# Performance work log

Measured on AMD Instinct MI355X. Metric: run time of the kernel, lower is better.

The kernel has to match this reference:

```python
import jax, jax.numpy as jnp
import numpy as np

# Module hyperparameters (init_kwargs)
N_CLASSES = 21
RADIUS = 5
SIZE = (256, 256)
SIGMA_DIST = 4.0
SIGMA_FEAT = 1.0
B, C = 8, 32


def _offsets(radius):
    """Integer (dy, dx) offsets with Euclidean distance < radius (includes (0,0))."""
    offs = []
    r = int(radius)
    for dy in range(-r + 1, r):
        for dx in range(-r + 1, r):
            if dy * dy + dx * dx < radius * radius:
                offs.append((dy, dx))
    return offs


OFFSETS = _offsets(RADIUS)  # 69 offsets for radius=5


def setup_inputs() -> dict:
    key = jax.random.key(0)
    k1, k2 = jax.random.split(key)
    H, W = SIZE
    classification = jax.random.uniform(k1, (B, N_CLASSES, H, W), dtype=jnp.float32)
    features = jax.random.normal(k2, (B, C, H, W), dtype=jnp.float32)
    return {"classification": classification, "features": features}


def reference(classification, features):
    # classification: [B, K, H, W] soft assignments S
    # features:       [B, C, H, W]
    Bb, K, H, W = classification.shape
    inv_sd2 = 1.0 / (SIGMA_DIST * SIGMA_DIST)
    inv_sf2 = 1.0 / (SIGMA_FEAT * SIGMA_FEAT)

    hs = jnp.arange(H)
    ws = jnp.arange(W)

    WS = jnp.zeros_like(classification)           # (W @ S), [B, K, H, W]
    degree = jnp.zeros((Bb, H, W), classification.dtype)

    # Loop over the small fixed set of neighbor offsets (69 for radius=5).
    for dy, dx in OFFSETS:
        f_nb = jnp.roll(features, (-dy, -dx), axis=(2, 3))
        s_nb = jnp.roll(classification, (-dy, -dx), axis=(2, 3))
        # mask out wrap-around: neighbor (h+dy, w+dx) must be in-bounds
        valid_h = (hs + dy >= 0) & (hs + dy < H)
        valid_w = (ws + dx >= 0) & (ws + dx < W)
        mask = (valid_h[:, None] & valid_w[None, :]).astype(classification.dtype)
        # Gaussian affinity: distance kernel * feature kernel
        feat_d2 = ((features - f_nb) ** 2).sum(axis=1)        # [B, H, W]
        w = jnp.exp(-(dy * dy + dx * dx) * inv_sd2 - feat_d2 * inv_sf2) * mask
        WS = WS + w[:, None] * s_nb
        degree = degree + w

    # numerator   = S^T W S : [B, K, K]
    # denominator = d^T S   : [B, K]
    num = jnp.einsum('bkhw,bjhw->bkj', classification, WS)
    den = jnp.einsum('bhw,bkhw->bk', degree, classification)
    return (num / den[:, None, :]).sum()
```

## Files before the change

kernel.cpp:

```cpp
#include <hip/hip_runtime.h>

#define HH 256
#define WW 256
#define HWPX 65536
#define BB 8
#define KK 21
#define CC 32
#define NT 8192
#define E_LOG2E 1.4426950408889634f
#define PEN -30000.0f

typedef _Float16 half2v __attribute__((ext_vector_type(2)));
typedef _Float16 half8  __attribute__((ext_vector_type(8)));
typedef float    f32x4v __attribute__((ext_vector_type(4)));
union F4H { float4 f4; half2v h[4]; half8 h8; };

__global__ __launch_bounds__(256) void prep(const float* __restrict__ cls,
                                            const float* __restrict__ feat,
                                            float4* __restrict__ fpk,
                                            float2* __restrict__ TN) {
    const int tid = blockIdx.x * 256 + threadIdx.x;
    const int b = tid >> 16;
    const int p = tid & (HWPX - 1);

    const float* cbase = cls + (size_t)b * KK * HWPX + p;
    float T = 0.f;
#pragma unroll
    for (int k = 0; k < KK; ++k) T += cbase[(size_t)k * HWPX];

    const float* src = feat + (size_t)b * CC * HWPX + p;
    float nq = 0.f;
#pragma unroll
    for (int j = 0; j < 4; ++j) {
        F4H u;
#pragma unroll
        for (int k = 0; k < 4; ++k) {
            float a  = src[(size_t)(j * 8 + 2 * k) * HWPX];
            float b2 = src[(size_t)(j * 8 + 2 * k + 1) * HWPX];
            u.h[k] = __builtin_bit_cast(half2v, __builtin_amdgcn_cvt_pkrtz(a, b2));
            nq = __builtin_amdgcn_fdot2(u.h[k], u.h[k], nq, false);
        }
        fpk[(size_t)j * (BB * HWPX) + tid] = u.f4;
    }
    TN[tid] = make_float2(T, nq);
}

__global__ __launch_bounds__(256) void affinity_mfma(const float4* __restrict__ fpk,
                                                     const float2* __restrict__ TN,
                                                     const float* __restrict__ cls,
                                                     float* __restrict__ partial) {
    __shared__ float smN[4][21], smD[4][21];
    const int L    = blockIdx.x;
    const int b    = L & 7;
    const int t    = L >> 3;
    const int xt   = t >> 6;
    const int ygrp = t & 63;
    const int wid  = threadIdx.x >> 6;
    const int lane = threadIdx.x & 63;
    const int g    = lane >> 4;
    const int c    = lane & 15;
    const int y    = ygrp * 4 + wid;
    const int x0   = xt * 16;

    const size_t bofs = (size_t)b * HWPX;
    const float4* fb  = fpk + bofs;
    const float2* tnb = TN + bofs;

    const int rowp = (y << 8) + x0;
    F4H afr; afr.f4 = fb[(size_t)g * (BB * HWPX) + rowp + c];

    float npE[4];
#pragma unroll
    for (int r = 0; r < 4; ++r) npE[r] = tnb[rowp + 4 * g + r].y * E_LOG2E;

    float cstA[2][4], cstB[2][4], cstC[2][4];
    int   voffF[2], voffT[2];
#pragma unroll
    for (int w = 0; w < 2; ++w) {
        const int w0  = w ? 12 : -4;
        const int xbu = x0 + w0 + c;
        const bool inb = (unsigned)xbu < WW;
        const int xbc = min(max(xbu, 0), WW - 1);
        voffF[w] = (g * (BB * HWPX) + xbc) * 16;
        voffT[w] = xbc * 8;
#pragma unroll
        for (int r = 0; r < 4; ++r) {
            const int dx = w0 + c - 4 * g - r;
            const int s2 = dx * dx;
            const float bp = fmaf((float)s2, -E_LOG2E / 16.f, -npE[r]);
            cstA[w][r] = (inb && s2 <= 16) ? bp : PEN;
            cstB[w][r] = (inb && s2 <= 9)  ? bp : PEN;
            cstC[w][r] = (inb && s2 <= 4)  ? bp : PEN;
        }
    }

    const f32x4v czero = {0.f, 0.f, 0.f, 0.f};
    float pdeg[4] = {0.f, 0.f, 0.f, 0.f};
    float pV[4]   = {0.f, 0.f, 0.f, 0.f};

    const char* fpkB = (const char*)fpk + bofs * 16;
    const char* tnB  = (const char*)TN + bofs * 8;

    auto body = [&](const float (&cst)[2][4], int ny, float cdy) {
        if ((unsigned)ny >= HH) return;
        const char* pF = fpkB + ((size_t)ny << 12);
        const char* pT = tnB  + ((size_t)ny << 11);
#pragma unroll
        for (int w = 0; w < 2; ++w) {
            F4H bfr; bfr.f4 = *(const float4*)(pF + voffF[w]);
            const float2 tq = *(const float2*)(pT + voffT[w]);
            f32x4v cz = __builtin_amdgcn_mfma_f32_16x16x32_f16(afr.h8, bfr.h8, czero, 0, 0, 0);
            const float t1 = fmaf(tq.y, -E_LOG2E, cdy);
#pragma unroll
            for (int r = 0; r < 4; ++r) {
                const float e2 = fmaf(cz[r], 2.f * E_LOG2E, cst[w][r] + t1);
                const float wv = __builtin_exp2f(e2);
                pdeg[r] += wv;
                pV[r]   = fmaf(wv, tq.x, pV[r]);
            }
        }
    };

#pragma unroll 1
    for (int d = -2; d <= 2; ++d)
        body(cstA, y + d, (float)(d * d) * (-E_LOG2E / 16.f));
    body(cstB, y - 3, 9.f  * (-E_LOG2E / 16.f));
    body(cstB, y + 3, 9.f  * (-E_LOG2E / 16.f));
    body(cstC, y - 4, 16.f * (-E_LOG2E / 16.f));
    body(cstC, y + 4, 16.f * (-E_LOG2E / 16.f));

#pragma unroll
    for (int m = 1; m <= 8; m <<= 1) {
#pragma unroll
        for (int r = 0; r < 4; ++r) {
            pdeg[r] += __shfl_xor(pdeg[r], m, 64);
            pV[r]   += __shfl_xor(pV[r], m, 64);
        }
    }

    float n0 = 0.f, d0 = 0.f, n1 = 0.f, d1 = 0.f;
    const float* clsb = cls + (size_t)b * KK * HWPX + rowp + 4 * g;
#pragma unroll
    for (int r = 0; r < 4; ++r) {
        const float s0 = clsb[(size_t)c * HWPX + r];
        n0 = fmaf(s0, pV[r], n0);
        d0 = fmaf(s0, pdeg[r], d0);
        if (c < 5) {
            const float s1 = clsb[(size_t)(c + 16) * HWPX + r];
            n1 = fmaf(s1, pV[r], n1);
            d1 = fmaf(s1, pdeg[r], d1);
        }
    }
#pragma unroll
    for (int m = 16; m <= 32; m <<= 1) {
        n0 += __shfl_xor(n0, m, 64);
        d0 += __shfl_xor(d0, m, 64);
        n1 += __shfl_xor(n1, m, 64);
        d1 += __shfl_xor(d1, m, 64);
    }
    if (lane < 16) {
        smN[wid][lane] = n0;
        smD[wid][lane] = d0;
        if (lane < 5) { smN[wid][16 + lane] = n1; smD[wid][16 + lane] = d1; }
    }
    __syncthreads();
    if (threadIdx.x < 2 * KK) {
        const int jq = threadIdx.x;
        const float v = (jq < KK)
            ? (smN[0][jq] + smN[1][jq] + smN[2][jq] + smN[3][jq])
            : (smD[0][jq - KK] + smD[1][jq - KK] + smD[2][jq - KK] + smD[3][jq - KK]);
        partial[(size_t)jq * NT + (size_t)b * 1024 + t] = v;
    }
}

__global__ __launch_bounds__(256) void reduce_part(const float* __restrict__ partial,
                                                   float* __restrict__ numer,
                                                   float* __restrict__ denom) {
    __shared__ float sm[4];
    const int jq = blockIdx.x;
    const int b  = blockIdx.y;
    const float* src = partial + (size_t)jq * NT + (size_t)b * 1024;
    float a = src[threadIdx.x] + src[threadIdx.x + 256]
            + src[threadIdx.x + 512] + src[threadIdx.x + 768];
#pragma unroll
    for (int off = 32; off > 0; off >>= 1) a += __shfl_down(a, off);
    if ((threadIdx.x & 63) == 0) sm[threadIdx.x >> 6] = a;
    __syncthreads();
    if (threadIdx.x == 0) {
        const float v = sm[0] + sm[1] + sm[2] + sm[3];
        if (jq < KK) numer[b * KK + jq] = v;
        else         denom[b * KK + jq - KK] = v;
    }
}

__global__ __launch_bounds__(256) void finalize(const float* __restrict__ numer,
                                                const float* __restrict__ denom,
                                                float* __restrict__ out) {
    __shared__ float sm[4];
    int i = threadIdx.x;
    float r = 0.f;
    if (i < BB * KK) r = numer[i] / denom[i];
#pragma unroll
    for (int off = 32; off > 0; off >>= 1) r += __shfl_down(r, off);
    if ((i & 63) == 0) sm[i >> 6] = r;
    __syncthreads();
    if (i == 0) out[0] = sm[0] + sm[1] + sm[2] + sm[3];
}

extern "C" void kernel_launch(void* const* d_in, const int* in_sizes, int n_in,
                              void* d_out, int out_size, void* d_ws, size_t ws_size,
                              hipStream_t stream) {
    const float* cls  = (const float*)d_in[0];
    const float* feat = (const float*)d_in[1];
    float* out = (float*)d_out;

    const size_t BHW = (size_t)BB * HWPX;
    float4* fpk     = (float4*)d_ws;
    float2* TN      = (float2*)((char*)d_ws + BHW * 64);
    float*  partial = (float*)((char*)TN + BHW * 8);
    float*  numer   = partial + (size_t)2 * KK * NT;
    float*  denom   = numer + BB * KK;

    prep<<<dim3((BB * HWPX) / 256), dim3(256), 0, stream>>>(cls, feat, fpk, TN);
    affinity_mfma<<<dim3(NT), dim3(256), 0, stream>>>(fpk, TN, cls, partial);
    reduce_part<<<dim3(2 * KK, BB), dim3(256), 0, stream>>>(partial, numer, denom);
    finalize<<<dim3(1), dim3(256), 0, stream>>>(numer, denom, out);
}
```

Before: 199.8 us.

## Retile affinity MFMA to 2x8 pixel tiles covering two rows per wave

```diff
diff --git a/kernel.cpp b/kernel.cpp
--- a/kernel.cpp
+++ b/kernel.cpp
@@ -53,45 +53,45 @@
     const int L    = blockIdx.x;
     const int b    = L & 7;
     const int t    = L >> 3;
-    const int xt   = t >> 6;
-    const int ygrp = t & 63;
     const int wid  = threadIdx.x >> 6;
     const int lane = threadIdx.x & 63;
     const int g    = lane >> 4;
     const int c    = lane & 15;
-    const int y    = ygrp * 4 + wid;
-    const int x0   = xt * 16;
+    const int idx  = t * 4 + wid;
+    const int y0   = (idx >> 5) * 2;
+    const int x0   = (idx & 31) * 8;
 
     const size_t bofs = (size_t)b * HWPX;
     const float4* fb  = fpk + bofs;
     const float2* tnb = TN + bofs;
 
-    const int rowp = (y << 8) + x0;
-    F4H afr; afr.f4 = fb[(size_t)g * (BB * HWPX) + rowp + c];
-
+    F4H afr;
+    afr.f4 = fb[(size_t)g * (BB * HWPX) + ((y0 + (c & 1)) << 8) + x0 + (c >> 1)];
+
+    int pxr[4];
     float npE[4];
 #pragma unroll
-    for (int r = 0; r < 4; ++r) npE[r] = tnb[rowp + 4 * g + r].y * E_LOG2E;
-
-    float cstA[2][4], cstB[2][4], cstC[2][4];
-    int   voffF[2], voffT[2];
-#pragma unroll
-    for (int w = 0; w < 2; ++w) {
-        const int w0  = w ? 12 : -4;
-        const int xbu = x0 + w0 + c;
-        const bool inb = (unsigned)xbu < WW;
-        const int xbc = min(max(xbu, 0), WW - 1);
-        voffF[w] = (g * (BB * HWPX) + xbc) * 16;
-        voffT[w] = xbc * 8;
-#pragma unroll
-        for (int r = 0; r < 4; ++r) {
-            const int dx = w0 + c - 4 * g - r;
-            const int s2 = dx * dx;
-            const float bp = fmaf((float)s2, -E_LOG2E / 16.f, -npE[r]);
-            cstA[w][r] = (inb && s2 <= 16) ? bp : PEN;
-            cstB[w][r] = (inb && s2 <= 9)  ? bp : PEN;
-            cstC[w][r] = (inb && s2 <= 4)  ? bp : PEN;
-        }
+    for (int r = 0; r < 4; ++r) {
+        pxr[r] = ((y0 + (r & 1)) << 8) + x0 + 2 * g + (r >> 1);
+        npE[r] = tnb[pxr[r]].y * E_LOG2E;
+    }
+
+    const int xbu  = x0 - 4 + c;
+    const bool inb = (unsigned)xbu < WW;
+    const int xbc  = min(max(xbu, 0), WW - 1);
+    const int voffF = (g * (BB * HWPX) + xbc) * 16;
+    const int voffT = xbc * 8;
+
+    float cst0[4], cst1[4], cst4[4], cst9[4], cst16[4];
+#pragma unroll
+    for (int r = 0; r < 4; ++r) {
+        const int dx = c - 4 - 2 * g - (r >> 1);
+        const int s2 = dx * dx;
+        cst0[r]  = (inb && s2 <= 16) ? fmaf((float)(s2 + 0),  -E_LOG2E / 16.f, -npE[r]) : PEN;
+        cst1[r]  = (inb && s2 <= 16) ? fmaf((float)(s2 + 1),  -E_LOG2E / 16.f, -npE[r]) : PEN;
+        cst4[r]  = (inb && s2 <= 16) ? fmaf((float)(s2 + 4),  -E_LOG2E / 16.f, -npE[r]) : PEN;
+        cst9[r]  = (inb && s2 <= 9)  ? fmaf((float)(s2 + 9),  -E_LOG2E / 16.f, -npE[r]) : PEN;
+        cst16[r] = (inb && s2 <= 4)  ? fmaf((float)(s2 + 16), -E_LOG2E / 16.f, -npE[r]) : PEN;
     }
 
     const f32x4v czero = {0.f, 0.f, 0.f, 0.f};
@@ -101,33 +101,42 @@
     const char* fpkB = (const char*)fpk + bofs * 16;
     const char* tnB  = (const char*)TN + bofs * 8;
 
-    auto body = [&](const float (&cst)[2][4], int ny, float cdy) {
+    auto body = [&](int ny, const float (&ce)[4], const float (&co)[4], int mode) {
         if ((unsigned)ny >= HH) return;
         const char* pF = fpkB + ((size_t)ny << 12);
         const char* pT = tnB  + ((size_t)ny << 11);
-#pragma unroll
-        for (int w = 0; w < 2; ++w) {
-            F4H bfr; bfr.f4 = *(const float4*)(pF + voffF[w]);
-            const float2 tq = *(const float2*)(pT + voffT[w]);
-            f32x4v cz = __builtin_amdgcn_mfma_f32_16x16x32_f16(afr.h8, bfr.h8, czero, 0, 0, 0);
-            const float t1 = fmaf(tq.y, -E_LOG2E, cdy);
-#pragma unroll
-            for (int r = 0; r < 4; ++r) {
-                const float e2 = fmaf(cz[r], 2.f * E_LOG2E, cst[w][r] + t1);
-                const float wv = __builtin_exp2f(e2);
-                pdeg[r] += wv;
-                pV[r]   = fmaf(wv, tq.x, pV[r]);
-            }
+        F4H bfr; bfr.f4 = *(const float4*)(pF + voffF);
+        const float2 tq = *(const float2*)(pT + voffT);
+        f32x4v cz = __builtin_amdgcn_mfma_f32_16x16x32_f16(afr.h8, bfr.h8, czero, 0, 0, 0);
+        const float t1 = tq.y * -E_LOG2E;
+        if (mode != 2) {
+            const float e0 = fmaf(cz[0], 2.f * E_LOG2E, ce[0] + t1);
+            const float w0 = __builtin_exp2f(e0);
+            pdeg[0] += w0;  pV[0] = fmaf(w0, tq.x, pV[0]);
+            const float e2 = fmaf(cz[2], 2.f * E_LOG2E, ce[2] + t1);
+            const float w2 = __builtin_exp2f(e2);
+            pdeg[2] += w2;  pV[2] = fmaf(w2, tq.x, pV[2]);
+        }
+        if (mode != 1) {
+            const float e1 = fmaf(cz[1], 2.f * E_LOG2E, co[1] + t1);
+            const float w1 = __builtin_exp2f(e1);
+            pdeg[1] += w1;  pV[1] = fmaf(w1, tq.x, pV[1]);
+            const float e3 = fmaf(cz[3], 2.f * E_LOG2E, co[3] + t1);
+            const float w3 = __builtin_exp2f(e3);
+            pdeg[3] += w3;  pV[3] = fmaf(w3, tq.x, pV[3]);
         }
     };
 
-#pragma unroll 1
-    for (int d = -2; d <= 2; ++d)
-        body(cstA, y + d, (float)(d * d) * (-E_LOG2E / 16.f));
-    body(cstB, y - 3, 9.f  * (-E_LOG2E / 16.f));
-    body(cstB, y + 3, 9.f  * (-E_LOG2E / 16.f));
-    body(cstC, y - 4, 16.f * (-E_LOG2E / 16.f));
-    body(cstC, y + 4, 16.f * (-E_LOG2E / 16.f));
+    body(y0 - 4, cst16, cst16, 1);
+    body(y0 - 3, cst9,  cst16, 0);
+    body(y0 - 2, cst4,  cst9,  0);
+    body(y0 - 1, cst1,  cst4,  0);
+    body(y0 + 0, cst0,  cst1,  0);
+    body(y0 + 1, cst1,  cst0,  0);
+    body(y0 + 2, cst4,  cst1,  0);
+    body(y0 + 3, cst9,  cst4,  0);
+    body(y0 + 4, cst16, cst9,  0);
+    body(y0 + 5, cst16, cst16, 2);
 
 #pragma unroll
     for (int m = 1; m <= 8; m <<= 1) {
@@ -139,14 +148,14 @@
     }
 
     float n0 = 0.f, d0 = 0.f, n1 = 0.f, d1 = 0.f;
-    const float* clsb = cls + (size_t)b * KK * HWPX + rowp + 4 * g;
+    const float* clsb = cls + (size_t)b * KK * HWPX;
 #pragma unroll
     for (int r = 0; r < 4; ++r) {
-        const float s0 = clsb[(size_t)c * HWPX + r];
+        const float s0 = clsb[(size_t)c * HWPX + pxr[r]];
         n0 = fmaf(s0, pV[r], n0);
         d0 = fmaf(s0, pdeg[r], d0);
         if (c < 5) {
-            const float s1 = clsb[(size_t)(c + 16) * HWPX + r];
+            const float s1 = clsb[(size_t)(c + 16) * HWPX + pxr[r]];
             n1 = fmaf(s1, pV[r], n1);
             d1 = fmaf(s1, pdeg[r], d1);
         }
```

Measured after the change: 179.0 us. -10.4%, faster.
